# Kernel optimization log

Measured on AMD Instinct MI355X. Metric: run time of the kernel, lower is better.

Reference implementation:

```python
import jax, jax.numpy as jnp
import numpy as np

K_NN = 16  # number of nearest neighbors (module init arg k)


def setup_inputs() -> dict:
    key = jax.random.key(0)
    k1, k2 = jax.random.split(key)
    xyz = jax.random.normal(k1, (8, 16384, 3), dtype=jnp.float32)
    centers = jax.random.normal(k2, (8, 1024, 3), dtype=jnp.float32)
    return {"xyz": xyz, "centers": centers}


def reference(xyz, centers):
    # avoiding the (B, N, K, 3) broadcast intermediate of the original while
    # computing the same torch.norm(xyz - centers, dim=-1) math.
    x_sq = jnp.sum(xyz * xyz, axis=-1)          # (B, N)
    c_sq = jnp.sum(centers * centers, axis=-1)  # (B, K)
    cross = jnp.einsum('bnd,bkd->bnk', xyz, centers)  # (B, N, K)
    d2 = x_sq[:, :, None] + c_sq[None if False else slice(None), None, :] - 2.0 * cross
    dist = jnp.sqrt(jnp.maximum(d2, 0.0))       # (B, N, K)
    # torch.topk(dist, k, dim=1, largest=False, sorted=True):
    # smallest-k over the N (points) axis, per center.
    neg = -jnp.transpose(dist, (0, 2, 1))       # (B, K, N)
    _, idx = jax.lax.top_k(neg, K_NN)           # (B, K, k), ascending distance
    return jnp.transpose(idx, (0, 2, 1))        # (B, k, K) to match torch dim=1 topk
```

## Files before the change

kernel.cpp:

```cpp
#include <hip/hip_runtime.h>
#include <stdint.h>

#define BB    8
#define NN    16384
#define KK    1024
#define KNN   16
#define QTR   (NN / 4)
#define QGRP  (QTR / 4)
#define PGRP  256
#define HCAP  96

typedef unsigned long long u64;

__device__ __forceinline__ u64 shfl_xor_u64(u64 v, int mask) {
    int lo = (int)(uint32_t)v;
    int hi = (int)(uint32_t)(v >> 32);
    lo = __shfl_xor(lo, mask, 64);
    hi = __shfl_xor(hi, mask, 64);
    return ((u64)(uint32_t)hi << 32) | (u64)(uint32_t)lo;
}

__device__ __forceinline__ u64 wave_min_u64(u64 v) {
#pragma unroll
    for (int off = 32; off > 0; off >>= 1) {
        u64 o = shfl_xor_u64(v, off);
        v = o < v ? o : v;
    }
    return v;
}

__device__ __forceinline__ float point_d2(const float* xb, int i,
                                          float c0, float c1, float c2, float csq) {
#pragma clang fp contract(off)
    float x0 = xb[i * 3 + 0];
    float x1 = xb[i * 3 + 1];
    float x2 = xb[i * 3 + 2];
    float xsq = (x0 * x0 + x1 * x1) + x2 * x2;
    float cross = __fmaf_rn(x2, c2, __fmaf_rn(x1, c1, x0 * c0));
    float d2 = (xsq + csq) - 2.0f * cross;
    return d2 < 0.0f ? 0.0f : d2;
}

__device__ __attribute__((noinline)) int fallback_scan(const float* xb,
                                                       float c0, float c1, float c2,
                                                       float csq, int lane) {
    u64 list[KNN];
#pragma unroll
    for (int j = 0; j < KNN; ++j) list[j] = ~0ull;
    for (int i = lane; i < NN; i += 64) {
        float d2 = point_d2(xb, i, c0, c1, c2, csq);
        float dist = __fsqrt_rn(d2);
        u64 key = ((u64)__float_as_uint(dist) << 32) | (u64)(uint32_t)i;
        if (key < list[KNN - 1]) {
#pragma unroll
            for (int j = 0; j < KNN; ++j) {
                bool lt = key < list[j];
                u64 lo = lt ? key : list[j];
                u64 hi = lt ? list[j] : key;
                list[j] = lo;
                key = hi;
            }
        }
    }
    int res = 0;
    for (int it = 0; it < KNN; ++it) {
        u64 best = wave_min_u64(list[0]);
        if (it == lane) res = (int)(uint32_t)best;
        if (list[0] == best) {
#pragma unroll
            for (int j = 0; j < KNN - 1; ++j) list[j] = list[j + 1];
            list[KNN - 1] = ~0ull;
        }
    }
    return res;
}

__device__ __forceinline__ float sixteenth_smallest(float m, int lane) {
    uint32_t u = __float_as_uint(m);
    uint32_t s = (u & 0x80000000u) ? ~u : (u | 0x80000000u);
    u64 v = ((u64)s << 32) | (unsigned)lane;
#pragma unroll
    for (int k = 2; k <= 64; k <<= 1) {
#pragma unroll
        for (int j = k >> 1; j > 0; j >>= 1) {
            u64 o = shfl_xor_u64(v, j);
            bool up = (lane & k) == 0;
            bool takeMin = ((lane & j) == 0) == up;
            u64 mn = v < o ? v : o;
            u64 mx = v < o ? o : v;
            v = takeMin ? mn : mx;
        }
    }
    uint32_t sb = (uint32_t)__shfl((int)(uint32_t)(v >> 32), 15, 64);
    uint32_t ub = (sb & 0x80000000u) ? (sb ^ 0x80000000u) : ~sb;
    return __uint_as_float(ub);
}

__device__ __forceinline__ void load_group(const float4* x4, int g,
                                           float (&px)[4], float (&py)[4],
                                           float (&pz)[4], float (&xs)[4]) {
#pragma clang fp contract(off)
    float4 f0 = x4[g * 3 + 0];
    float4 f1 = x4[g * 3 + 1];
    float4 f2 = x4[g * 3 + 2];
    px[0] = f0.x; py[0] = f0.y; pz[0] = f0.z;
    px[1] = f0.w; py[1] = f1.x; pz[1] = f1.y;
    px[2] = f1.z; py[2] = f1.w; pz[2] = f2.x;
    px[3] = f2.y; py[3] = f2.z; pz[3] = f2.w;
#pragma unroll
    for (int k = 0; k < 4; ++k)
        xs[k] = (px[k] * px[k] + py[k] * py[k]) + pz[k] * pz[k];
}

__global__ __launch_bounds__(256, 8) void knn_kernel(const float* __restrict__ xyz,
                                                     const float* __restrict__ centers,
                                                     int* __restrict__ out) {
#pragma clang fp contract(off)
    const int q = (int)(threadIdx.x >> 6);
    const int lane = (int)(threadIdx.x & 63);
    const int cbase = (int)blockIdx.x * 4;
    const int b = cbase >> 10;

    __shared__ float    s_min[4][256];
    __shared__ float    s_T[4];
    __shared__ int      s_cnt[4][4];
    __shared__ uint32_t s_idx[4][4][HCAP];

    const float n0[3] = { -2.0f * centers[(cbase + 0) * 3 + 0],
                          -2.0f * centers[(cbase + 0) * 3 + 1],
                          -2.0f * centers[(cbase + 0) * 3 + 2] };
    const float n1[3] = { -2.0f * centers[(cbase + 1) * 3 + 0],
                          -2.0f * centers[(cbase + 1) * 3 + 1],
                          -2.0f * centers[(cbase + 1) * 3 + 2] };
    const float n2[3] = { -2.0f * centers[(cbase + 2) * 3 + 0],
                          -2.0f * centers[(cbase + 2) * 3 + 1],
                          -2.0f * centers[(cbase + 2) * 3 + 2] };
    const float n3[3] = { -2.0f * centers[(cbase + 3) * 3 + 0],
                          -2.0f * centers[(cbase + 3) * 3 + 1],
                          -2.0f * centers[(cbase + 3) * 3 + 2] };

    const float* xb = xyz + (size_t)b * NN * 3;
    const float4* x4 = (const float4*)xb;
    const int gbase = q * QGRP;

    float m0 = __builtin_inff(), m1 = m0, m2 = m0, m3 = m0;
#pragma unroll 2
    for (int s = 0; s < PGRP / 64; ++s) {
        int g = gbase + s * 64 + lane;
        float px[4], py[4], pz[4], xs[4];
        load_group(x4, g, px, py, pz, xs);
#pragma unroll
        for (int k = 0; k < 4; ++k) {
            float d0 = __fmaf_rn(px[k], n0[0], __fmaf_rn(py[k], n0[1], __fmaf_rn(pz[k], n0[2], xs[k])));
            float d1 = __fmaf_rn(px[k], n1[0], __fmaf_rn(py[k], n1[1], __fmaf_rn(pz[k], n1[2], xs[k])));
            float d2 = __fmaf_rn(px[k], n2[0], __fmaf_rn(py[k], n2[1], __fmaf_rn(pz[k], n2[2], xs[k])));
            float d3 = __fmaf_rn(px[k], n3[0], __fmaf_rn(py[k], n3[1], __fmaf_rn(pz[k], n3[2], xs[k])));
            m0 = d0 < m0 ? d0 : m0;
            m1 = d1 < m1 ? d1 : m1;
            m2 = d2 < m2 ? d2 : m2;
            m3 = d3 < m3 ? d3 : m3;
        }
    }
    s_min[0][q * 64 + lane] = m0;
    s_min[1][q * 64 + lane] = m1;
    s_min[2][q * 64 + lane] = m2;
    s_min[3][q * 64 + lane] = m3;
    if (threadIdx.x < 16) s_cnt[threadIdx.x >> 2][threadIdx.x & 3] = 0;
    __syncthreads();
    {
        float v = fminf(fminf(s_min[q][lane], s_min[q][64 + lane]),
                        fminf(s_min[q][128 + lane], s_min[q][192 + lane]));
        float t = sixteenth_smallest(v, lane);
        if (lane == 0) s_T[q] = t;
    }
    __syncthreads();
    const float T0 = s_T[0], T1 = s_T[1], T2 = s_T[2], T3 = s_T[3];
    const float U0 = T0 + fabsf(T0) * 1e-5f + 5e-4f;
    const float U1 = T1 + fabsf(T1) * 1e-5f + 5e-4f;
    const float U2 = T2 + fabsf(T2) * 1e-5f + 5e-4f;
    const float U3 = T3 + fabsf(T3) * 1e-5f + 5e-4f;

#pragma unroll 2
    for (int s = 0; s < QGRP / 64; ++s) {
        int g = gbase + s * 64 + lane;
        float px[4], py[4], pz[4], xs[4];
        load_group(x4, g, px, py, pz, xs);
#pragma unroll
        for (int k = 0; k < 4; ++k) {
            float d0 = __fmaf_rn(px[k], n0[0], __fmaf_rn(py[k], n0[1], __fmaf_rn(pz[k], n0[2], xs[k])));
            float d1 = __fmaf_rn(px[k], n1[0], __fmaf_rn(py[k], n1[1], __fmaf_rn(pz[k], n1[2], xs[k])));
            float d2 = __fmaf_rn(px[k], n2[0], __fmaf_rn(py[k], n2[1], __fmaf_rn(pz[k], n2[2], xs[k])));
            float d3 = __fmaf_rn(px[k], n3[0], __fmaf_rn(py[k], n3[1], __fmaf_rn(pz[k], n3[2], xs[k])));
            int i = g * 4 + k;
            if (d0 <= U0) {
                int pos = atomicAdd(&s_cnt[0][q], 1);
                if (pos < HCAP) s_idx[0][q][pos] = (uint32_t)i;
            }
            if (d1 <= U1) {
                int pos = atomicAdd(&s_cnt[1][q], 1);
                if (pos < HCAP) s_idx[1][q][pos] = (uint32_t)i;
            }
            if (d2 <= U2) {
                int pos = atomicAdd(&s_cnt[2][q], 1);
                if (pos < HCAP) s_idx[2][q][pos] = (uint32_t)i;
            }
            if (d3 <= U3) {
                int pos = atomicAdd(&s_cnt[3][q], 1);
                if (pos < HCAP) s_idx[3][q][pos] = (uint32_t)i;
            }
        }
    }
    __syncthreads();

    const int cc = cbase + q;
    const float c0 = centers[cc * 3 + 0];
    const float c1 = centers[cc * 3 + 1];
    const float c2 = centers[cc * 3 + 2];
    const float csq = (c0 * c0 + c1 * c1) + c2 * c2;
    const int k0 = s_cnt[q][0], k1 = s_cnt[q][1], k2 = s_cnt[q][2], k3 = s_cnt[q][3];
    const int p1o = k0, p2o = k0 + k1, p3o = k0 + k1 + k2;
    const int total = p3o + k3;
    const bool ok = (k0 <= HCAP) & (k1 <= HCAP) & (k2 <= HCAP) & (k3 <= HCAP) &
                    (total <= 4 * 64);

    int res = 0;
    if (ok) {
        u64 l0 = ~0ull, l1 = ~0ull, l2 = ~0ull, l3 = ~0ull;
        for (int j = lane; j < total; j += 64) {
            int qq, off;
            if (j < p1o)      { qq = 0; off = j; }
            else if (j < p2o) { qq = 1; off = j - p1o; }
            else if (j < p3o) { qq = 2; off = j - p2o; }
            else              { qq = 3; off = j - p3o; }
            int idx = (int)s_idx[q][qq][off];
            float d2 = point_d2(xb, idx, c0, c1, c2, csq);
            u64 key = ((u64)__float_as_uint(__fsqrt_rn(d2)) << 32) | (u64)(uint32_t)idx;
            bool t;
            t = key < l0; { u64 lo = t ? key : l0, hi = t ? l0 : key; l0 = lo; key = hi; }
            t = key < l1; { u64 lo = t ? key : l1, hi = t ? l1 : key; l1 = lo; key = hi; }
            t = key < l2; { u64 lo = t ? key : l2, hi = t ? l2 : key; l2 = lo; key = hi; }
            t = key < l3; { u64 lo = t ? key : l3, hi = t ? l3 : key; l3 = lo; key = hi; }
        }
        for (int it = 0; it < KNN; ++it) {
            u64 best = wave_min_u64(l0);
            if (it == lane) res = (int)(uint32_t)best;
            if (l0 == best) { l0 = l1; l1 = l2; l2 = l3; l3 = ~0ull; }
        }
    } else {
        res = fallback_scan(xb, c0, c1, c2, csq, lane);
    }

    if (lane < KNN) {
        out[((size_t)b * KNN + lane) * KK + (cc & 1023)] = res;
    }
}

extern "C" void kernel_launch(void* const* d_in, const int* in_sizes, int n_in,
                              void* d_out, int out_size, void* d_ws, size_t ws_size,
                              hipStream_t stream) {
    const float* xyz = (const float*)d_in[0];
    const float* centers = (const float*)d_in[1];
    int* out = (int*)d_out;
    (void)d_ws; (void)ws_size;

    const int nblocks = BB * KK / 4;
    hipLaunchKernelGGL(knn_kernel, dim3(nblocks), dim3(256), 0, stream,
                       xyz, centers, out);
}
```

Before: 99.28 us.

## Process eight centers per 512-thread block and replace serial top-k extraction with bitonic sorts

Each block now handles eight centers with eight waves sharing the point scan, so every loaded point is reused against twice as many centers. Candidate buffers are merged into one shared list per center with capacity 256. The threshold-estimation prepass now covers 128 groups per wave instead of 256. The final 16-step wave-min extraction is replaced by a bitonic sort of per-lane heads, a gather of the top 16 lanes' four-entry lists, and a second 64-wide sort. Register pressure from eight centers and the larger block could lower occupancy, and a looser threshold sample may push more centers onto the fallback path.

```diff
diff --git a/kernel.cpp b/kernel.cpp
--- a/kernel.cpp
+++ b/kernel.cpp
@@ -5,10 +5,11 @@
 #define NN    16384
 #define KK    1024
 #define KNN   16
-#define QTR   (NN / 4)
-#define QGRP  (QTR / 4)
-#define PGRP  256
-#define HCAP  96
+#define CPB   8
+#define WPB   8
+#define EGRP  (NN / 4 / WPB)
+#define PGRP  128
+#define TCAP  256
 
 typedef unsigned long long u64;
 
@@ -20,6 +21,12 @@
     return ((u64)(uint32_t)hi << 32) | (u64)(uint32_t)lo;
 }
 
+__device__ __forceinline__ u64 shfl_u64(u64 v, int src) {
+    int lo = __shfl((int)(uint32_t)v, src, 64);
+    int hi = __shfl((int)(uint32_t)(v >> 32), src, 64);
+    return ((u64)(uint32_t)hi << 32) | (u64)(uint32_t)lo;
+}
+
 __device__ __forceinline__ u64 wave_min_u64(u64 v) {
 #pragma unroll
     for (int off = 32; off > 0; off >>= 1) {
@@ -27,6 +34,35 @@
         v = o < v ? o : v;
     }
     return v;
+}
+
+__device__ __forceinline__ void sort64_kv(u64& key, uint32_t& pay, int lane) {
+#pragma unroll
+    for (int k = 2; k <= 64; k <<= 1) {
+#pragma unroll
+        for (int j = k >> 1; j > 0; j >>= 1) {
+            u64 okey = shfl_xor_u64(key, j);
+            uint32_t opay = (uint32_t)__shfl_xor((int)pay, j, 64);
+            bool tmin = ((lane & j) == 0) == ((lane & k) == 0);
+            bool osm = okey < key;
+            bool take = tmin ? osm : !osm;
+            if (take) { key = okey; pay = opay; }
+        }
+    }
+}
+
+__device__ __forceinline__ void sort64_k(u64& key, int lane) {
+#pragma unroll
+    for (int k = 2; k <= 64; k <<= 1) {
+#pragma unroll
+        for (int j = k >> 1; j > 0; j >>= 1) {
+            u64 okey = shfl_xor_u64(key, j);
+            bool tmin = ((lane & j) == 0) == ((lane & k) == 0);
+            bool osm = okey < key;
+            bool take = tmin ? osm : !osm;
+            if (take) key = okey;
+        }
+    }
 }
 
 __device__ __forceinline__ float point_d2(const float* xb, int i,
@@ -112,101 +148,87 @@
         xs[k] = (px[k] * px[k] + py[k] * py[k]) + pz[k] * pz[k];
 }
 
-__global__ __launch_bounds__(256, 8) void knn_kernel(const float* __restrict__ xyz,
+__global__ __launch_bounds__(512, 4) void knn_kernel(const float* __restrict__ xyz,
                                                      const float* __restrict__ centers,
                                                      int* __restrict__ out) {
 #pragma clang fp contract(off)
     const int q = (int)(threadIdx.x >> 6);
     const int lane = (int)(threadIdx.x & 63);
-    const int cbase = (int)blockIdx.x * 4;
+    const int cbase = (int)blockIdx.x * CPB;
     const int b = cbase >> 10;
 
-    __shared__ float    s_min[4][256];
-    __shared__ float    s_T[4];
-    __shared__ int      s_cnt[4][4];
-    __shared__ uint32_t s_idx[4][4][HCAP];
-
-    const float n0[3] = { -2.0f * centers[(cbase + 0) * 3 + 0],
-                          -2.0f * centers[(cbase + 0) * 3 + 1],
-                          -2.0f * centers[(cbase + 0) * 3 + 2] };
-    const float n1[3] = { -2.0f * centers[(cbase + 1) * 3 + 0],
-                          -2.0f * centers[(cbase + 1) * 3 + 1],
-                          -2.0f * centers[(cbase + 1) * 3 + 2] };
-    const float n2[3] = { -2.0f * centers[(cbase + 2) * 3 + 0],
-                          -2.0f * centers[(cbase + 2) * 3 + 1],
-                          -2.0f * centers[(cbase + 2) * 3 + 2] };
-    const float n3[3] = { -2.0f * centers[(cbase + 3) * 3 + 0],
-                          -2.0f * centers[(cbase + 3) * 3 + 1],
-                          -2.0f * centers[(cbase + 3) * 3 + 2] };
+    __shared__ float    s_min[CPB][512];
+    __shared__ float    s_T[CPB];
+    __shared__ int      s_cnt[CPB];
+    __shared__ uint32_t s_idx[CPB][TCAP];
+
+    float n[CPB][3];
+#pragma unroll
+    for (int c = 0; c < CPB; ++c) {
+        n[c][0] = -2.0f * centers[(cbase + c) * 3 + 0];
+        n[c][1] = -2.0f * centers[(cbase + c) * 3 + 1];
+        n[c][2] = -2.0f * centers[(cbase + c) * 3 + 2];
+    }
 
     const float* xb = xyz + (size_t)b * NN * 3;
     const float4* x4 = (const float4*)xb;
-    const int gbase = q * QGRP;
-
-    float m0 = __builtin_inff(), m1 = m0, m2 = m0, m3 = m0;
-#pragma unroll 2
+    const int gbase = q * EGRP;
+
+    float m[CPB];
+#pragma unroll
+    for (int c = 0; c < CPB; ++c) m[c] = __builtin_inff();
+#pragma unroll
     for (int s = 0; s < PGRP / 64; ++s) {
         int g = gbase + s * 64 + lane;
         float px[4], py[4], pz[4], xs[4];
         load_group(x4, g, px, py, pz, xs);
 #pragma unroll
         for (int k = 0; k < 4; ++k) {
-            float d0 = __fmaf_rn(px[k], n0[0], __fmaf_rn(py[k], n0[1], __fmaf_rn(pz[k], n0[2], xs[k])));
-            float d1 = __fmaf_rn(px[k], n1[0], __fmaf_rn(py[k], n1[1], __fmaf_rn(pz[k], n1[2], xs[k])));
-            float d2 = __fmaf_rn(px[k], n2[0], __fmaf_rn(py[k], n2[1], __fmaf_rn(pz[k], n2[2], xs[k])));
-            float d3 = __fmaf_rn(px[k], n3[0], __fmaf_rn(py[k], n3[1], __fmaf_rn(pz[k], n3[2], xs[k])));
-            m0 = d0 < m0 ? d0 : m0;
-            m1 = d1 < m1 ? d1 : m1;
-            m2 = d2 < m2 ? d2 : m2;
-            m3 = d3 < m3 ? d3 : m3;
-        }
-    }
-    s_min[0][q * 64 + lane] = m0;
-    s_min[1][q * 64 + lane] = m1;
-    s_min[2][q * 64 + lane] = m2;
-    s_min[3][q * 64 + lane] = m3;
-    if (threadIdx.x < 16) s_cnt[threadIdx.x >> 2][threadIdx.x & 3] = 0;
+#pragma unroll
+            for (int c = 0; c < CPB; ++c) {
+                float d = __fmaf_rn(px[k], n[c][0],
+                          __fmaf_rn(py[k], n[c][1],
+                          __fmaf_rn(pz[k], n[c][2], xs[k])));
+                m[c] = d < m[c] ? d : m[c];
+            }
+        }
+    }
+#pragma unroll
+    for (int c = 0; c < CPB; ++c) s_min[c][threadIdx.x] = m[c];
+    if (threadIdx.x < CPB) s_cnt[threadIdx.x] = 0;
     __syncthreads();
     {
-        float v = fminf(fminf(s_min[q][lane], s_min[q][64 + lane]),
-                        fminf(s_min[q][128 + lane], s_min[q][192 + lane]));
+        float v = s_min[q][lane];
+#pragma unroll
+        for (int w = 1; w < WPB; ++w) v = fminf(v, s_min[q][w * 64 + lane]);
         float t = sixteenth_smallest(v, lane);
         if (lane == 0) s_T[q] = t;
     }
     __syncthreads();
-    const float T0 = s_T[0], T1 = s_T[1], T2 = s_T[2], T3 = s_T[3];
-    const float U0 = T0 + fabsf(T0) * 1e-5f + 5e-4f;
-    const float U1 = T1 + fabsf(T1) * 1e-5f + 5e-4f;
-    const float U2 = T2 + fabsf(T2) * 1e-5f + 5e-4f;
-    const float U3 = T3 + fabsf(T3) * 1e-5f + 5e-4f;
+    float U[CPB];
+#pragma unroll
+    for (int c = 0; c < CPB; ++c) {
+        float T = s_T[c];
+        U[c] = T + fabsf(T) * 1e-5f + 5e-4f;
+    }
 
 #pragma unroll 2
-    for (int s = 0; s < QGRP / 64; ++s) {
+    for (int s = 0; s < EGRP / 64; ++s) {
         int g = gbase + s * 64 + lane;
         float px[4], py[4], pz[4], xs[4];
         load_group(x4, g, px, py, pz, xs);
 #pragma unroll
         for (int k = 0; k < 4; ++k) {
-            float d0 = __fmaf_rn(px[k], n0[0], __fmaf_rn(py[k], n0[1], __fmaf_rn(pz[k], n0[2], xs[k])));
-            float d1 = __fmaf_rn(px[k], n1[0], __fmaf_rn(py[k], n1[1], __fmaf_rn(pz[k], n1[2], xs[k])));
-            float d2 = __fmaf_rn(px[k], n2[0], __fmaf_rn(py[k], n2[1], __fmaf_rn(pz[k], n2[2], xs[k])));
-            float d3 = __fmaf_rn(px[k], n3[0], __fmaf_rn(py[k], n3[1], __fmaf_rn(pz[k], n3[2], xs[k])));
             int i = g * 4 + k;
-            if (d0 <= U0) {
-                int pos = atomicAdd(&s_cnt[0][q], 1);
-                if (pos < HCAP) s_idx[0][q][pos] = (uint32_t)i;
-            }
-            if (d1 <= U1) {
-                int pos = atomicAdd(&s_cnt[1][q], 1);
-                if (pos < HCAP) s_idx[1][q][pos] = (uint32_t)i;
-            }
-            if (d2 <= U2) {
-                int pos = atomicAdd(&s_cnt[2][q], 1);
-                if (pos < HCAP) s_idx[2][q][pos] = (uint32_t)i;
-            }
-            if (d3 <= U3) {
-                int pos = atomicAdd(&s_cnt[3][q], 1);
-                if (pos < HCAP) s_idx[3][q][pos] = (uint32_t)i;
+#pragma unroll
+            for (int c = 0; c < CPB; ++c) {
+                float d = __fmaf_rn(px[k], n[c][0],
+                          __fmaf_rn(py[k], n[c][1],
+                          __fmaf_rn(pz[k], n[c][2], xs[k])));
+                if (d <= U[c]) {
+                    int pos = atomicAdd(&s_cnt[c], 1);
+                    if (pos < TCAP) s_idx[c][pos] = (uint32_t)i;
+                }
             }
         }
     }
@@ -217,22 +239,13 @@
     const float c1 = centers[cc * 3 + 1];
     const float c2 = centers[cc * 3 + 2];
     const float csq = (c0 * c0 + c1 * c1) + c2 * c2;
-    const int k0 = s_cnt[q][0], k1 = s_cnt[q][1], k2 = s_cnt[q][2], k3 = s_cnt[q][3];
-    const int p1o = k0, p2o = k0 + k1, p3o = k0 + k1 + k2;
-    const int total = p3o + k3;
-    const bool ok = (k0 <= HCAP) & (k1 <= HCAP) & (k2 <= HCAP) & (k3 <= HCAP) &
-                    (total <= 4 * 64);
-
-    int res = 0;
-    if (ok) {
+    const int total = s_cnt[q];
+
+    uint32_t outIdx;
+    if (total <= TCAP) {
         u64 l0 = ~0ull, l1 = ~0ull, l2 = ~0ull, l3 = ~0ull;
         for (int j = lane; j < total; j += 64) {
-            int qq, off;
-            if (j < p1o)      { qq = 0; off = j; }
-            else if (j < p2o) { qq = 1; off = j - p1o; }
-            else if (j < p3o) { qq = 2; off = j - p2o; }
-            else              { qq = 3; off = j - p3o; }
-            int idx = (int)s_idx[q][qq][off];
+            int idx = (int)s_idx[q][j];
             float d2 = point_d2(xb, idx, c0, c1, c2, csq);
             u64 key = ((u64)__float_as_uint(__fsqrt_rn(d2)) << 32) | (u64)(uint32_t)idx;
             bool t;
@@ -241,17 +254,24 @@
             t = key < l2; { u64 lo = t ? key : l2, hi = t ? l2 : key; l2 = lo; key = hi; }
             t = key < l3; { u64 lo = t ? key : l3, hi = t ? l3 : key; l3 = lo; key = hi; }
         }
-        for (int it = 0; it < KNN; ++it) {
-            u64 best = wave_min_u64(l0);
-            if (it == lane) res = (int)(uint32_t)best;
-            if (l0 == best) { l0 = l1; l1 = l2; l2 = l3; l3 = ~0ull; }
-        }
+        u64 key = l0;
+        uint32_t pay = (uint32_t)lane;
+        sort64_kv(key, pay, lane);
+        int pos = lane >> 2, elem = lane & 3;
+        int sid = __shfl((int)pay, pos, 64);
+        u64 g0 = shfl_u64(l0, sid);
+        u64 g1 = shfl_u64(l1, sid);
+        u64 g2 = shfl_u64(l2, sid);
+        u64 g3 = shfl_u64(l3, sid);
+        u64 gk = (elem == 0) ? g0 : (elem == 1) ? g1 : (elem == 2) ? g2 : g3;
+        sort64_k(gk, lane);
+        outIdx = (uint32_t)gk;
     } else {
-        res = fallback_scan(xb, c0, c1, c2, csq, lane);
+        outIdx = (uint32_t)fallback_scan(xb, c0, c1, c2, csq, lane);
     }
 
     if (lane < KNN) {
-        out[((size_t)b * KNN + lane) * KK + (cc & 1023)] = res;
+        out[((size_t)b * KNN + lane) * KK + (cc & 1023)] = (int)outIdx;
     }
 }
 
@@ -263,7 +283,7 @@
     int* out = (int*)d_out;
     (void)d_ws; (void)ws_size;
 
-    const int nblocks = BB * KK / 4;
-    hipLaunchKernelGGL(knn_kernel, dim3(nblocks), dim3(256), 0, stream,
+    const int nblocks = BB * KK / CPB;
+    hipLaunchKernelGGL(knn_kernel, dim3(nblocks), dim3(512), 0, stream,
                        xyz, centers, out);
 }
```

Result: slower. 103.8 us (+4.6%).
